# Performance work log

Hardware: AMD Instinct MI355X
Metric: run time of the kernel (lower is better)

## Reference

```python
import jax, jax.numpy as jnp
import numpy as np

N_NODES = 50000
N_EDGES = 800000
F_IN = 64
H1 = 64
H2 = 64
OUT = 8
N_GRAPHS = 128


def gcn_conv(x, W, b, src, dst, n_nodes):
    """PyG GCNConv: sym-normalized aggregation with self-loops.
    out_i = sum_{j->i} d_j^{-1/2} d_i^{-1/2} (x_j W) + d_i^{-1} (x_i W) + b
    where d includes the self-loop (+1)."""
    h = x @ W  # [N, out]
    ones = jnp.ones((src.shape[0],), dtype=x.dtype)
    deg = jnp.zeros((n_nodes,), dtype=x.dtype).at[dst].add(ones) + 1.0  # +1 self-loop
    dinv_sqrt = jax.lax.rsqrt(deg)
    norm = dinv_sqrt[src] * dinv_sqrt[dst]  # [E]
    msgs = h[src] * norm[:, None]  # [E, out] -- dominant memory traffic
    agg = jax.ops.segment_sum(msgs, dst, num_segments=n_nodes)
    agg = agg + h * (1.0 / deg)[:, None]  # self-loop term (norm = 1/d_i)
    return agg + b


def setup_inputs() -> dict:
    key = jax.random.key(0)
    ks = jax.random.split(key, 10)
    x = jax.random.normal(ks[0], (N_NODES, F_IN), dtype=jnp.float32)
    src = jax.random.randint(ks[1], (N_EDGES,), 0, N_NODES, dtype=jnp.int32)
    dst = jax.random.randint(ks[2], (N_EDGES,), 0, N_NODES, dtype=jnp.int32)
    batch = jnp.sort(jax.random.randint(ks[3], (N_NODES,), 0, N_GRAPHS, dtype=jnp.int32))
    s1 = 1.0 / np.sqrt(F_IN)
    s2 = 1.0 / np.sqrt(H1)
    s3 = 1.0 / np.sqrt(H2)
    W1 = jax.random.uniform(ks[4], (F_IN, H1), jnp.float32, -s1, s1)
    b1 = jnp.zeros((H1,), jnp.float32)
    W2 = jax.random.uniform(ks[5], (H1, H2), jnp.float32, -s2, s2)
    b2 = jnp.zeros((H2,), jnp.float32)
    Wfc = jax.random.uniform(ks[6], (H2, OUT), jnp.float32, -s3, s3)
    bfc = jax.random.uniform(ks[7], (OUT,), jnp.float32, -s3, s3)
    return {"x": x, "src": src, "dst": dst, "batch": batch,
            "W1": W1, "b1": b1, "W2": W2, "b2": b2, "Wfc": Wfc, "bfc": bfc}


def reference(x, src, dst, batch, W1, b1, W2, b2, Wfc, bfc):
    n = x.shape[0]
    h = jnp.tanh(gcn_conv(x, W1, b1, src, dst, n))  # dropout(p=0) is identity
    h = jnp.tanh(gcn_conv(h, W2, b2, src, dst, n))
    # global mean pool over graphs
    sums = jax.ops.segment_sum(h, batch, num_segments=N_GRAPHS)  # [G, H2]
    counts = jax.ops.segment_sum(jnp.ones((n,), h.dtype), batch, num_segments=N_GRAPHS)
    pooled = sums / jnp.maximum(counts, 1.0)[:, None]
    return pooled @ Wfc + bfc  # [G, OUT]
```

## Files before the change

kernel.cpp:

```cpp
#include <hip/hip_runtime.h>
#include <hip/hip_fp16.h>
#include <math.h>


#define TPB 256
#define NBIN 256
#define NBLK 256
#define MSZ  (NBIN*NBLK)
#define CAP  4608

#define ADD8(a, v) do { const __half2* _h = (const __half2*)&(v);             \
    float2 _f0 = __half22float2(_h[0]), _f1 = __half22float2(_h[1]);          \
    float2 _f2 = __half22float2(_h[2]), _f3 = __half22float2(_h[3]);          \
    a[0] += _f0.x; a[1] += _f0.y; a[2] += _f1.x; a[3] += _f1.y;               \
    a[4] += _f2.x; a[5] += _f2.y; a[6] += _f3.x; a[7] += _f3.y; } while (0)

__global__ __launch_bounds__(TPB) void k_hist_gemm(const int* __restrict__ dst, int E,
                                                   int* __restrict__ Gh, int binw,
                                                   const float* __restrict__ X,
                                                   const float* __restrict__ W,
                                                   float* __restrict__ Y, int N) {
    if (blockIdx.x < NBIN) {
        __shared__ int hist[NBIN];
        hist[threadIdx.x] = 0;
        __syncthreads();
        int chunk = (E + NBLK - 1) / NBLK;
        int start = blockIdx.x * chunk;
        int end = min(start + chunk, E);
        for (int e = start + threadIdx.x; e < end; e += TPB)
            atomicAdd(&hist[dst[e] / binw], 1);
        __syncthreads();
        Gh[threadIdx.x * NBLK + blockIdx.x] = hist[threadIdx.x];
        return;
    }
    __shared__ float4 Ws[64][16];
    for (int i = threadIdx.x; i < 64 * 16; i += TPB)
        Ws[i >> 4][i & 15] = ((const float4*)W)[i];
    __syncthreads();

    int row = (blockIdx.x - NBIN) * TPB + threadIdx.x;
    if (row >= N) return;
    float xr[64];
    const float4* xp = (const float4*)(X + (size_t)row * 64);
#pragma unroll
    for (int q = 0; q < 16; q++) {
        float4 t = xp[q];
        xr[4 * q + 0] = t.x; xr[4 * q + 1] = t.y;
        xr[4 * q + 2] = t.z; xr[4 * q + 3] = t.w;
    }
    float4 acc[16];
#pragma unroll
    for (int q = 0; q < 16; q++) acc[q] = make_float4(0.f, 0.f, 0.f, 0.f);
#pragma unroll
    for (int k = 0; k < 64; k++) {
        float xk = xr[k];
#pragma unroll
        for (int q = 0; q < 16; q++) {
            float4 w = Ws[k][q];
            acc[q].x += xk * w.x; acc[q].y += xk * w.y;
            acc[q].z += xk * w.z; acc[q].w += xk * w.w;
        }
    }
    float4* yp = (float4*)(Y + (size_t)row * 64);
#pragma unroll
    for (int q = 0; q < 16; q++) yp[q] = acc[q];
}

__global__ __launch_bounds__(1024) void k_scan(const int* __restrict__ Gh,
                                               int* __restrict__ Gbase,
                                               int* __restrict__ binptr, int E) {
    __shared__ int buf[1024];
    __shared__ int bprefix;
    int blk = blockIdx.x;

    int limit = blk * 1024;
    int part = 0;
    for (int j = threadIdx.x; j < limit; j += 1024) part += Gh[j];
    buf[threadIdx.x] = part;
    __syncthreads();
#pragma unroll
    for (int off = 512; off > 0; off >>= 1) {
        if (threadIdx.x < off) buf[threadIdx.x] += buf[threadIdx.x + off];
        __syncthreads();
    }
    if (threadIdx.x == 0) bprefix = buf[0];
    __syncthreads();

    int i = blk * 1024 + threadIdx.x;
    int v = Gh[i];
    buf[threadIdx.x] = v;
    __syncthreads();
#pragma unroll
    for (int off = 1; off < 1024; off <<= 1) {
        int t = (threadIdx.x >= off) ? buf[threadIdx.x - off] : 0;
        __syncthreads();
        buf[threadIdx.x] += t;
        __syncthreads();
    }
    int r = buf[threadIdx.x] - v + bprefix;
    Gbase[i] = r;
    if ((i & (NBLK - 1)) == 0) binptr[i / NBLK] = r;
    if (i == 0) binptr[NBIN] = E;
}

__global__ __launch_bounds__(TPB) void k_binscatter(const int* __restrict__ src,
                                                    const int* __restrict__ dst,
                                                    const int* __restrict__ Gbase,
                                                    unsigned int* __restrict__ Ebin,
                                                    int E, int binw) {
    __shared__ int curs[NBIN];
    curs[threadIdx.x] = Gbase[threadIdx.x * NBLK + blockIdx.x];
    __syncthreads();
    int chunk = (E + NBLK - 1) / NBLK;
    int start = blockIdx.x * chunk;
    int end = min(start + chunk, E);
    for (int e = start + threadIdx.x; e < end; e += TPB) {
        int d = dst[e], s = src[e];
        int pos = atomicAdd(&curs[d / binw], 1);
        Ebin[pos] = ((unsigned)d << 16) | (unsigned)s;
    }
}

__global__ __launch_bounds__(1024) void k_binsort(const unsigned int* __restrict__ Ebin,
                                                  const int* __restrict__ binptr,
                                                  int* __restrict__ rowptr,
                                                  int* __restrict__ eidx,
                                                  float* __restrict__ ds,
                                                  const float* __restrict__ A,
                                                  __half* __restrict__ Ah,
                                                  int N, int E, int binw) {
    __shared__ unsigned int eLDS[CAP];
    __shared__ int outLDS[CAP];
    __shared__ int hist[NBIN];
    __shared__ int scanb[NBIN];
    __shared__ int curs[NBIN];

    int b = blockIdx.x;
    int base = binptr[b];
    int cntE = min(binptr[b + 1] - base, CAP);
    int nodeBase = b * binw;

    if (threadIdx.x < NBIN) hist[threadIdx.x] = 0;
    __syncthreads();

    for (int j = threadIdx.x; j < cntE; j += 1024) {
        unsigned int u = Ebin[base + j];
        eLDS[j] = u;
        atomicAdd(&hist[(int)(u >> 16) - nodeBase], 1);
    }
    __syncthreads();

    int v = 0;
    if (threadIdx.x < NBIN) { v = hist[threadIdx.x]; scanb[threadIdx.x] = v; }
    __syncthreads();
#pragma unroll
    for (int off = 1; off < NBIN; off <<= 1) {
        int t = (threadIdx.x < NBIN && threadIdx.x >= off) ? scanb[threadIdx.x - off] : 0;
        __syncthreads();
        if (threadIdx.x < NBIN) scanb[threadIdx.x] += t;
        __syncthreads();
    }
    if (threadIdx.x < NBIN) {
        int excl = scanb[threadIdx.x] - v;
        curs[threadIdx.x] = excl;
        int node = nodeBase + threadIdx.x;
        if (threadIdx.x < binw && node < N) {
            rowptr[node] = base + excl;
            ds[node] = rsqrtf((float)v + 1.0f);
        }
    }
    if (b == NBIN - 1 && threadIdx.x == 0) rowptr[N] = E;
    __syncthreads();

    for (int j = threadIdx.x; j < cntE; j += 1024) {
        unsigned int u = eLDS[j];
        int p = atomicAdd(&curs[(int)(u >> 16) - nodeBase], 1);
        outLDS[p] = (int)(u & 0xFFFFu);
    }
    __syncthreads();
    for (int j = threadIdx.x; j < cntE; j += 1024)
        eidx[base + j] = outLDS[j];

    const float2* A2 = (const float2*)A;
    __half2* Ah2 = (__half2*)Ah;
    int total = binw * 32;
    for (int j = threadIdx.x; j < total; j += 1024) {
        int li = j >> 5;
        int node = nodeBase + li;
        if (node >= N) continue;
        float s = rsqrtf((float)hist[li] + 1.0f);
        int c2 = j & 31;
        float2 t = A2[(size_t)node * 32 + c2];
        Ah2[(size_t)node * 32 + c2] = __float22half2_rn(make_float2(t.x * s, t.y * s));
    }
}

__global__ __launch_bounds__(TPB) void k_agg8h(const float4* __restrict__ Hp,
                                               float4* __restrict__ Oh,
                                               const int* __restrict__ rowptr,
                                               const int* __restrict__ eidx,
                                               const float* __restrict__ ds,
                                               const float* __restrict__ b, int N) {
    int wid = (blockIdx.x * TPB + threadIdx.x) >> 6;
    int lane = threadIdx.x & 63;
    if (wid >= N) return;
    int r = lane >> 3;
    int c = lane & 7;

    int lo = rowptr[wid], hi = rowptr[wid + 1];
    float a[8] = {0.f, 0.f, 0.f, 0.f, 0.f, 0.f, 0.f, 0.f};

    int base = lo;
    for (; base + 16 <= hi; base += 16) {
        int s0 = eidx[base + r], s1 = eidx[base + 8 + r];
        float4 v0 = Hp[(size_t)s0 * 8 + c];
        float4 v1 = Hp[(size_t)s1 * 8 + c];
        ADD8(a, v0);
        ADD8(a, v1);
    }
    if (base + 8 <= hi) {
        int s0 = eidx[base + r];
        float4 v0 = Hp[(size_t)s0 * 8 + c];
        ADD8(a, v0);
        base += 8;
    }
    int rem = hi - base;
    if (r < rem) {
        int s0 = eidx[base + r];
        float4 v0 = Hp[(size_t)s0 * 8 + c];
        ADD8(a, v0);
    }

#pragma unroll
    for (int j = 0; j < 8; j++) a[j] += __shfl_xor(a[j], 8);
#pragma unroll
    for (int j = 0; j < 8; j++) a[j] += __shfl_xor(a[j], 16);
#pragma unroll
    for (int j = 0; j < 8; j++) a[j] += __shfl_xor(a[j], 32);

    if (r == 0) {
        float4 sv = Hp[(size_t)wid * 8 + c];
        ADD8(a, sv);
        float dsd = ds[wid];
        float4 bb0 = ((const float4*)b)[c * 2];
        float4 bb1 = ((const float4*)b)[c * 2 + 1];
        float o0 = tanhf(a[0] * dsd + bb0.x);
        float o1 = tanhf(a[1] * dsd + bb0.y);
        float o2 = tanhf(a[2] * dsd + bb0.z);
        float o3 = tanhf(a[3] * dsd + bb0.w);
        float o4 = tanhf(a[4] * dsd + bb1.x);
        float o5 = tanhf(a[5] * dsd + bb1.y);
        float o6 = tanhf(a[6] * dsd + bb1.z);
        float o7 = tanhf(a[7] * dsd + bb1.w);
        float4 pk;
        __half2* ph = (__half2*)&pk;
        ph[0] = __float22half2_rn(make_float2(o0, o1));
        ph[1] = __float22half2_rn(make_float2(o2, o3));
        ph[2] = __float22half2_rn(make_float2(o4, o5));
        ph[3] = __float22half2_rn(make_float2(o6, o7));
        Oh[(size_t)wid * 8 + c] = pk;
    }
}

__global__ __launch_bounds__(TPB) void k_gemm64h(const __half* __restrict__ Xh,
                                                 const float* __restrict__ W,
                                                 __half* __restrict__ Ah, int N,
                                                 const float* __restrict__ ds) {
    __shared__ float4 Ws[64][16];
    for (int i = threadIdx.x; i < 64 * 16; i += TPB)
        Ws[i >> 4][i & 15] = ((const float4*)W)[i];
    __syncthreads();

    int row = blockIdx.x * TPB + threadIdx.x;
    if (row >= N) return;
    float xr[64];
    const float4* xp = (const float4*)(Xh + (size_t)row * 64);
#pragma unroll
    for (int q = 0; q < 8; q++) {
        float4 t = xp[q];
        const __half2* h = (const __half2*)&t;
        float2 f0 = __half22float2(h[0]), f1 = __half22float2(h[1]);
        float2 f2 = __half22float2(h[2]), f3 = __half22float2(h[3]);
        xr[8 * q + 0] = f0.x; xr[8 * q + 1] = f0.y;
        xr[8 * q + 2] = f1.x; xr[8 * q + 3] = f1.y;
        xr[8 * q + 4] = f2.x; xr[8 * q + 5] = f2.y;
        xr[8 * q + 6] = f3.x; xr[8 * q + 7] = f3.y;
    }
    float4 acc[16];
#pragma unroll
    for (int q = 0; q < 16; q++) acc[q] = make_float4(0.f, 0.f, 0.f, 0.f);
#pragma unroll
    for (int k = 0; k < 64; k++) {
        float xk = xr[k];
#pragma unroll
        for (int q = 0; q < 16; q++) {
            float4 w = Ws[k][q];
            acc[q].x += xk * w.x; acc[q].y += xk * w.y;
            acc[q].z += xk * w.z; acc[q].w += xk * w.w;
        }
    }
    float s = ds[row];
    __half2* yh = (__half2*)(Ah + (size_t)row * 64);
#pragma unroll
    for (int q = 0; q < 16; q++) {
        yh[2 * q]     = __float22half2_rn(make_float2(acc[q].x * s, acc[q].y * s));
        yh[2 * q + 1] = __float22half2_rn(make_float2(acc[q].z * s, acc[q].w * s));
    }
}

__global__ __launch_bounds__(TPB) void k_poolfc(const __half* __restrict__ H,
                                                const int* __restrict__ batch,
                                                const float* __restrict__ Wfc,
                                                const float* __restrict__ bfc,
                                                float* __restrict__ out, int N) {
    int g = blockIdx.x;
    __shared__ int range[2];
    __shared__ float red[4][64];
    if (threadIdx.x == 0) {
        int lo = 0, hi = N;
        while (lo < hi) { int m = (lo + hi) >> 1; if (batch[m] < g) lo = m + 1; else hi = m; }
        range[0] = lo;
        hi = N;
        while (lo < hi) { int m = (lo + hi) >> 1; if (batch[m] < g + 1) lo = m + 1; else hi = m; }
        range[1] = lo;
    }
    __syncthreads();
    int lo = range[0], hi = range[1];
    int wid = threadIdx.x >> 6, lane = threadIdx.x & 63;

    float acc = 0.0f;
    for (int n = lo + wid; n < hi; n += 4) acc += __half2float(H[(size_t)n * 64 + lane]);
    red[wid][lane] = acc;
    __syncthreads();
    if (wid == 0) {
        float s = red[0][lane] + red[1][lane] + red[2][lane] + red[3][lane];
        float cgt = fmaxf((float)(hi - lo), 1.0f);
        red[0][lane] = s / cgt;
    }
    __syncthreads();
    if (threadIdx.x < 8) {
        int o = threadIdx.x;
        float accf = bfc[o];
#pragma unroll
        for (int f = 0; f < 64; f++) accf += red[0][f] * Wfc[f * 8 + o];
        out[g * 8 + o] = accf;
    }
}

extern "C" void kernel_launch(void* const* d_in, const int* in_sizes, int n_in,
                              void* d_out, int out_size, void* d_ws, size_t ws_size,
                              hipStream_t stream) {
    const float* x     = (const float*)d_in[0];
    const int*   src   = (const int*)d_in[1];
    const int*   dst   = (const int*)d_in[2];
    const int*   batch = (const int*)d_in[3];
    const float* W1    = (const float*)d_in[4];
    const float* b1    = (const float*)d_in[5];
    const float* W2    = (const float*)d_in[6];
    const float* b2    = (const float*)d_in[7];
    const float* Wfc   = (const float*)d_in[8];
    const float* bfc   = (const float*)d_in[9];
    float* out = (float*)d_out;

    const int N = in_sizes[0] / 64;
    const int E = in_sizes[1];
    const int G = out_size / 8;
    const int binw = (N + NBIN - 1) / NBIN;

    const size_t NB = (size_t)N * 64 * sizeof(float);
    char* ws = (char*)d_ws;
    size_t off = 0;
    float*  A    = (float*)(ws + off);  off += NB;
    __half* Ah   = (__half*)(ws + off); off += NB / 2;
    __half* Bh   = (__half*)(ws + off); off += NB / 2;
    unsigned int* Ebin = (unsigned int*)Bh;
    __half* B2h  = (__half*)(ws + off); off += NB / 2;
    int*   eidx   = (int*)(ws + off);   off += (size_t)E * 4;
    int*   Gh     = (int*)(ws + off);   off += (size_t)MSZ * 4;
    int*   Gbase  = (int*)(ws + off);   off += (size_t)MSZ * 4;
    int*   binptr = (int*)(ws + off);   off += (size_t)(NBIN + 1) * 4;
    int*   rowptr = (int*)(ws + off);   off += (size_t)(N + 1) * 4;
    float* dsv    = (float*)(ws + off); off += (size_t)N * 4;

    const int gN = (N + TPB - 1) / TPB;
    const int gW = (N * 64 + TPB - 1) / TPB;

    k_hist_gemm<<<NBIN + gN, TPB, 0, stream>>>(dst, E, Gh, binw, x, W1, A, N);
    k_scan<<<MSZ / 1024, 1024, 0, stream>>>(Gh, Gbase, binptr, E);
    k_binscatter<<<NBLK, TPB, 0, stream>>>(src, dst, Gbase, Ebin, E, binw);
    k_binsort<<<NBIN, 1024, 0, stream>>>(Ebin, binptr, rowptr, eidx, dsv, A, Ah, N, E, binw);

    k_agg8h<<<gW, TPB, 0, stream>>>((const float4*)Ah, (float4*)Bh, rowptr, eidx, dsv, b1, N);
    k_gemm64h<<<gN, TPB, 0, stream>>>(Bh, W2, Ah, N, dsv);
    k_agg8h<<<gW, TPB, 0, stream>>>((const float4*)Ah, (float4*)B2h, rowptr, eidx, dsv, b2, N);
    k_poolfc<<<G, TPB, 0, stream>>>(B2h, batch, Wfc, bfc, out, N);
}
```

Measured before the change: 163.3 us.

## Fuse layer-1 aggregation with layer-2 GEMM in one wavefront-per-node kernel

```diff
diff --git a/kernel.cpp b/kernel.cpp
--- a/kernel.cpp
+++ b/kernel.cpp
@@ -193,6 +193,80 @@
         float2 t = A2[(size_t)node * 32 + c2];
         Ah2[(size_t)node * 32 + c2] = __float22half2_rn(make_float2(t.x * s, t.y * s));
     }
+}
+
+__global__ __launch_bounds__(TPB) void k_agg_gemm(const float4* __restrict__ Hp,
+                                                  __half* __restrict__ H2,
+                                                  const int* __restrict__ rowptr,
+                                                  const int* __restrict__ eidx,
+                                                  const float* __restrict__ ds,
+                                                  const float* __restrict__ b1,
+                                                  const float* __restrict__ W2,
+                                                  int N) {
+    __shared__ float W2s[64 * 64];
+    __shared__ float bs[64];
+    for (int i = threadIdx.x; i < 64 * 16; i += TPB)
+        ((float4*)W2s)[i] = ((const float4*)W2)[i];
+    if (threadIdx.x < 64) bs[threadIdx.x] = b1[threadIdx.x];
+    __syncthreads();
+
+    int wid = (blockIdx.x * TPB + threadIdx.x) >> 6;
+    int lane = threadIdx.x & 63;
+    if (wid >= N) return;
+    int r = lane >> 3;
+    int c = lane & 7;
+
+    int lo = rowptr[wid], hi = rowptr[wid + 1];
+    float a[8] = {0.f, 0.f, 0.f, 0.f, 0.f, 0.f, 0.f, 0.f};
+
+    int base = lo;
+    for (; base + 16 <= hi; base += 16) {
+        int s0 = eidx[base + r], s1 = eidx[base + 8 + r];
+        float4 v0 = Hp[(size_t)s0 * 8 + c];
+        float4 v1 = Hp[(size_t)s1 * 8 + c];
+        ADD8(a, v0);
+        ADD8(a, v1);
+    }
+    if (base + 8 <= hi) {
+        int s0 = eidx[base + r];
+        float4 v0 = Hp[(size_t)s0 * 8 + c];
+        ADD8(a, v0);
+        base += 8;
+    }
+    int rem = hi - base;
+    if (r < rem) {
+        int s0 = eidx[base + r];
+        float4 v0 = Hp[(size_t)s0 * 8 + c];
+        ADD8(a, v0);
+    }
+    if (r == 0) {
+        float4 sv = Hp[(size_t)wid * 8 + c];
+        ADD8(a, sv);
+    }
+
+#pragma unroll
+    for (int j = 0; j < 8; j++) a[j] += __shfl_xor(a[j], 8);
+#pragma unroll
+    for (int j = 0; j < 8; j++) a[j] += __shfl_xor(a[j], 16);
+#pragma unroll
+    for (int j = 0; j < 8; j++) a[j] += __shfl_xor(a[j], 32);
+
+    float dsd = ds[wid];
+    float t[8];
+#pragma unroll
+    for (int j = 0; j < 8; j++)
+        t[j] = tanhf(a[j] * dsd + bs[c * 8 + j]);
+
+    float acc = 0.0f;
+#pragma unroll
+    for (int cp = 0; cp < 8; cp++) {
+#pragma unroll
+        for (int j = 0; j < 8; j++) {
+            float rf = __shfl(t[j], cp);
+            acc += rf * W2s[(cp * 8 + j) * 64 + lane];
+        }
+    }
+    H2[(size_t)wid * 64 + lane] = __float2half_rn(acc * dsd);
 }
 
 __global__ __launch_bounds__(TPB) void k_agg8h(const float4* __restrict__ Hp,
@@ -262,52 +336,6 @@
     }
 }
 
-__global__ __launch_bounds__(TPB) void k_gemm64h(const __half* __restrict__ Xh,
-                                                 const float* __restrict__ W,
-                                                 __half* __restrict__ Ah, int N,
-                                                 const float* __restrict__ ds) {
-    __shared__ float4 Ws[64][16];
-    for (int i = threadIdx.x; i < 64 * 16; i += TPB)
-        Ws[i >> 4][i & 15] = ((const float4*)W)[i];
-    __syncthreads();
-
-    int row = blockIdx.x * TPB + threadIdx.x;
-    if (row >= N) return;
-    float xr[64];
-    const float4* xp = (const float4*)(Xh + (size_t)row * 64);
-#pragma unroll
-    for (int q = 0; q < 8; q++) {
-        float4 t = xp[q];
-        const __half2* h = (const __half2*)&t;
-        float2 f0 = __half22float2(h[0]), f1 = __half22float2(h[1]);
-        float2 f2 = __half22float2(h[2]), f3 = __half22float2(h[3]);
-        xr[8 * q + 0] = f0.x; xr[8 * q + 1] = f0.y;
-        xr[8 * q + 2] = f1.x; xr[8 * q + 3] = f1.y;
-        xr[8 * q + 4] = f2.x; xr[8 * q + 5] = f2.y;
-        xr[8 * q + 6] = f3.x; xr[8 * q + 7] = f3.y;
-    }
-    float4 acc[16];
-#pragma unroll
-    for (int q = 0; q < 16; q++) acc[q] = make_float4(0.f, 0.f, 0.f, 0.f);
-#pragma unroll
-    for (int k = 0; k < 64; k++) {
-        float xk = xr[k];
-#pragma unroll
-        for (int q = 0; q < 16; q++) {
-            float4 w = Ws[k][q];
-            acc[q].x += xk * w.x; acc[q].y += xk * w.y;
-            acc[q].z += xk * w.z; acc[q].w += xk * w.w;
-        }
-    }
-    float s = ds[row];
-    __half2* yh = (__half2*)(Ah + (size_t)row * 64);
-#pragma unroll
-    for (int q = 0; q < 16; q++) {
-        yh[2 * q]     = __float22half2_rn(make_float2(acc[q].x * s, acc[q].y * s));
-        yh[2 * q + 1] = __float22half2_rn(make_float2(acc[q].z * s, acc[q].w * s));
-    }
-}
-
 __global__ __launch_bounds__(TPB) void k_poolfc(const __half* __restrict__ H,
                                                 const int* __restrict__ batch,
                                                 const float* __restrict__ Wfc,
@@ -372,9 +400,9 @@
     size_t off = 0;
     float*  A    = (float*)(ws + off);  off += NB;
     __half* Ah   = (__half*)(ws + off); off += NB / 2;
-    __half* Bh   = (__half*)(ws + off); off += NB / 2;
-    unsigned int* Ebin = (unsigned int*)Bh;
+    __half* A2h  = (__half*)(ws + off); off += NB / 2;
     __half* B2h  = (__half*)(ws + off); off += NB / 2;
+    unsigned int* Ebin = (unsigned int*)B2h;
     int*   eidx   = (int*)(ws + off);   off += (size_t)E * 4;
     int*   Gh     = (int*)(ws + off);   off += (size_t)MSZ * 4;
     int*   Gbase  = (int*)(ws + off);   off += (size_t)MSZ * 4;
@@ -390,8 +418,7 @@
     k_binscatter<<<NBLK, TPB, 0, stream>>>(src, dst, Gbase, Ebin, E, binw);
     k_binsort<<<NBIN, 1024, 0, stream>>>(Ebin, binptr, rowptr, eidx, dsv, A, Ah, N, E, binw);
 
-    k_agg8h<<<gW, TPB, 0, stream>>>((const float4*)Ah, (float4*)Bh, rowptr, eidx, dsv, b1, N);
-    k_gemm64h<<<gN, TPB, 0, stream>>>(Bh, W2, Ah, N, dsv);
-    k_agg8h<<<gW, TPB, 0, stream>>>((const float4*)Ah, (float4*)B2h, rowptr, eidx, dsv, b2, N);
+    k_agg_gemm<<<gW, TPB, 0, stream>>>((const float4*)Ah, A2h, rowptr, eidx, dsv, b1, W2, N);
+    k_agg8h<<<gW, TPB, 0, stream>>>((const float4*)A2h, (float4*)B2h, rowptr, eidx, dsv, b2, N);
     k_poolfc<<<G, TPB, 0, stream>>>(B2h, batch, Wfc, bfc, out, N);
 }
```

New measurement: 182.3 us. +11.6%, slower.
